# Kernel tuning notes

Measured on AMD Instinct MI355X. Metric: run time of the kernel, lower is better.

The kernel has to match this reference:

```python
import jax, jax.numpy as jnp
import numpy as np

B, L, H, E = 2, 2048, 8, 64
S = L  # self-attention


def setup_inputs() -> dict:
    key = jax.random.key(0)
    k1, k2, k3, k4, k5 = jax.random.split(key, 5)
    return {
        "queries": jax.random.normal(k1, (B, L, H, E), dtype=jnp.float32),
        "keys": jax.random.normal(k2, (B, S, H, E), dtype=jnp.float32),
        "values": jax.random.normal(k3, (B, S, H, E), dtype=jnp.float32),
        "tau": jax.random.uniform(k4, (B, 1), dtype=jnp.float32),
        "delta": jax.random.normal(k5, (B, S), dtype=jnp.float32),
    }


def reference(queries, keys, values, tau, delta):
    # De-stationary attention: scores = (QK^T) * tau + delta, causal mask, softmax, AV
    E_ = queries.shape[-1]
    scale = 1.0 / jnp.sqrt(jnp.float32(E_))
    tau_b = tau[:, None, None, :]      # [B,1,1,1]
    delta_b = delta[:, None, None, :]  # [B,1,1,S]
    scores = jnp.einsum('blhe,bshe->bhls', queries, keys) * tau_b + delta_b  # [B,H,L,S]
    Lq, Sk = scores.shape[-2], scores.shape[-1]
    causal = jnp.triu(jnp.ones((Lq, Sk), dtype=bool), k=1)  # True = masked
    scores = jnp.where(causal[None, None], -jnp.inf, scores)
    A = jax.nn.softmax(scale * scores, axis=-1)
    V = jnp.einsum('bhls,bshd->blhd', A, values)
    return V
```

## Files before the change

### kernel.cpp

```cpp
#include <hip/hip_runtime.h>


typedef _Float16 h8 __attribute__((ext_vector_type(8)));
typedef _Float16 h2 __attribute__((ext_vector_type(2)));
typedef float f32x4 __attribute__((ext_vector_type(4)));

constexpr int Bc = 2, Lc = 2048, Hc = 8, Ec = 64, Sc = 2048;
constexpr int QTL = 128;
constexpr int NQT = Lc / QTL;
constexpr int KT = 64;
constexpr int NBH = Bc * Hc;
constexpr int CH = 8;
constexpr int EPB = 40;
constexpr int NIT = NBH * EPB;
constexpr float SCALE = 0.125f;
constexpr float LOG2E = 1.44269504088896340736f;

__constant__ int d_qtbase[16] = {0,1,2,3,4,6,8,10,12,15,18,21,24,28,32,36};
__constant__ signed char d_eqt[40] = {
  15,15,15,15,
  14,14,14,
  13,13,13,
  12,12,12,
  11,11,11,
  10,10,
   9, 9,
   8, 8,
   7, 7,
   6,
   5,
   4,
   3,
  14,10, 6, 2,
  13, 9, 5, 1,
  12, 8, 4, 0};
__constant__ signed char d_ec0[40] = {
   0, 1, 2, 3,
   0, 1, 2,
   0, 1, 2,
   0, 1, 2,
   0, 1, 2,
   0, 1,
   0, 1,
   0, 1,
   0, 1,
   0,
   0,
   0,
   0,
   3, 2, 1, 0,
   3, 2, 1, 0,
   3, 2, 1, 0};

__device__ __forceinline__ h2 pk2(float x, float y) {
  return __builtin_bit_cast(h2, __builtin_amdgcn_cvt_pkrtz(x, y));
}
template <int CTRL>
__device__ __forceinline__ float dpp_f(float x) {
  int r = __builtin_amdgcn_update_dpp(0, __builtin_bit_cast(int, x), CTRL, 0xF, 0xF, true);
  return __builtin_bit_cast(float, r);
}
__device__ __forceinline__ void gl16(const void* g, void* l) {
  __builtin_amdgcn_global_load_lds(
      (const __attribute__((address_space(1))) void*)g,
      (__attribute__((address_space(3))) void*)l, 16, 0, 0);
}

__global__ __launch_bounds__(256, 4)
void dsattn_prep(const float* __restrict__ Kg, const float* __restrict__ Vg,
                 _Float16* __restrict__ Kh, _Float16* __restrict__ Vh) {
  __shared__ __align__(16) _Float16 T[64][72];
  const int kt = (int)blockIdx.x;
  const int bh = (int)blockIdx.y;
  const int b = bh >> 3, h = bh & 7;
  const int tid = (int)threadIdx.x;
  const int sr = tid >> 2;
  const int e0 = (tid & 3) << 4;
  const int s = kt * KT + sr;

  {
    const float* kp = Kg + (((size_t)b * Sc + s) * Hc + h) * Ec + e0;
    float4 a0 = ((const float4*)kp)[0], a1 = ((const float4*)kp)[1];
    float4 a2 = ((const float4*)kp)[2], a3 = ((const float4*)kp)[3];
    union { h8 v; h2 c[4]; } u0, u1;
    u0.c[0] = pk2(a0.x, a0.y); u0.c[1] = pk2(a0.z, a0.w);
    u0.c[2] = pk2(a1.x, a1.y); u0.c[3] = pk2(a1.z, a1.w);
    u1.c[0] = pk2(a2.x, a2.y); u1.c[1] = pk2(a2.z, a2.w);
    u1.c[2] = pk2(a3.x, a3.y); u1.c[3] = pk2(a3.z, a3.w);
    char* out = (char*)Kh + (((size_t)bh * Sc + s) << 7);
    const int sl = e0 >> 3;
    const int rx = (sr & 7) << 4;
    *(h8*)(out + ((sl << 4) ^ rx)) = u0.v;
    *(h8*)(out + (((sl + 1) << 4) ^ rx)) = u1.v;
  }

  {
    const float* vp = Vg + (((size_t)b * Sc + s) * Hc + h) * Ec + e0;
    float4 v0 = ((const float4*)vp)[0], v1 = ((const float4*)vp)[1];
    float4 v2 = ((const float4*)vp)[2], v3 = ((const float4*)vp)[3];
    const float ev[16] = {v0.x, v0.y, v0.z, v0.w, v1.x, v1.y, v1.z, v1.w,
                          v2.x, v2.y, v2.z, v2.w, v3.x, v3.y, v3.z, v3.w};
#pragma unroll
    for (int j = 0; j < 8; ++j) {
      h2 t = pk2(ev[2 * j], ev[2 * j + 1]);
      T[e0 + 2 * j][sr] = t[0];
      T[e0 + 2 * j + 1][sr] = t[1];
    }
  }
  __syncthreads();
  {
    const int er = tid >> 2;
    const int k0 = (tid & 3) << 4;
    h8 w0 = *(const h8*)&T[er][k0];
    h8 w1 = *(const h8*)&T[er][k0 + 8];
    char* out = (char*)Vh + (((size_t)bh * 32 + kt) << 13) + er * 128;
    const int sl = k0 >> 3;
    const int rx = (er & 7) << 4;
    *(h8*)(out + ((sl << 4) ^ rx)) = w0;
    *(h8*)(out + (((sl + 1) << 4) ^ rx)) = w1;
  }
}

__global__ __launch_bounds__(256, 3)
void dsattn_fwd_main(const float* __restrict__ Qg, const _Float16* __restrict__ Kh,
                     const _Float16* __restrict__ Vh, const float* __restrict__ taug,
                     const float* __restrict__ deltag, float* __restrict__ Og,
                     _Float16* __restrict__ Opart, float* __restrict__ Lpart) {
  __shared__ __align__(16) _Float16 Ks[2][KT * 64];
  __shared__ __align__(16) _Float16 Vt[2][Ec * 64];
  __shared__ __align__(16) _Float16 Pb[4][16 * 64];

  const int tid = (int)threadIdx.x;
  const int wave = tid >> 6, lane = tid & 63;
  const int quad = lane >> 4, l16 = lane & 15;
  _Float16* pb = &Pb[wave][0];
  const int lo = l16 & 1;
  const int pbase = (lo ? 32 : 0) + (l16 & ~1);
  const int kx = (l16 & 7) << 3;
  const int koff0 = (quad * 8) ^ kx;
  const int koff1 = (quad * 8 + 32) ^ kx;

  h8 onesf;
#pragma unroll
  for (int j = 0; j < 8; ++j) onesf[j] = (_Float16)1.0f;

  for (int it = (int)blockIdx.x; it < NIT; it += (int)gridDim.x) {
    const int xcd = it & 7;
    const int r_ = it >> 3;
    const int bh = (xcd << 1) | (r_ & 1);
    const int e = r_ >> 1;
    const int qt = d_eqt[e], c0 = d_ec0[e];
    const int ntiles = 2 * qt + 2;
    const int nch = (ntiles + CH - 1) / CH;
    const int ktBeg = c0 * CH;
    const int ktEnd = min(ktBeg + CH - 1, ntiles - 1);
    const int q0 = qt * QTL;
    const int b = bh >> 3, h = bh & 7;
    const float ct = taug[b] * (SCALE * LOG2E);

    h8 qfrag[2][2];
#pragma unroll
    for (int f = 0; f < 2; ++f)
#pragma unroll
      for (int kk = 0; kk < 2; ++kk) {
        const float* qp = Qg + (((size_t)b * Lc + q0 + 32 * wave + 16 * f + l16) * Hc + h) * Ec
                         + quad * 8 + kk * 32;
        const float4* p = (const float4*)qp;
        union { h8 v; h2 c[4]; } u;
        float4 a0 = p[0], a1 = p[1];
        u.c[0] = pk2(a0.x, a0.y); u.c[1] = pk2(a0.z, a0.w);
        u.c[2] = pk2(a1.x, a1.y); u.c[3] = pk2(a1.z, a1.w);
        qfrag[f][kk] = u.v;
      }

    f32x4 Oacc[2][4], Osum[2];
#pragma unroll
    for (int f = 0; f < 2; ++f) {
#pragma unroll
      for (int nt = 0; nt < 4; ++nt) Oacc[f][nt] = (f32x4){0.f, 0.f, 0.f, 0.f};
      Osum[f] = (f32x4){0.f, 0.f, 0.f, 0.f};
    }
    float dcur[4];

    __syncthreads();

    {
      const char* kg = (const char*)Kh + (((size_t)bh * Sc + (size_t)ktBeg * KT) << 7)
                       + wave * 2048 + lane * 16;
      const char* vg = (const char*)Vh + (((size_t)bh * 32 + ktBeg) << 13)
                       + wave * 2048 + lane * 16;
      char* kl = (char*)&Ks[0][0] + wave * 2048;
      char* vl = (char*)&Vt[0][0] + wave * 2048;
      gl16(kg, kl); gl16(kg + 1024, kl + 1024);
      gl16(vg, vl); gl16(vg + 1024, vl + 1024);
#pragma unroll
      for (int nt = 0; nt < 4; ++nt)
        dcur[nt] = deltag[(size_t)b * Sc + ktBeg * KT + nt * 16 + l16] * (SCALE * LOG2E);
    }

    for (int kt = ktBeg; kt <= ktEnd; ++kt) {
      const int cur = (kt - ktBeg) & 1;
      const bool pf = (kt < ktEnd);
      const int kbase = kt * KT;

      __syncthreads();

      float dn[4];
      if (pf) {
        const char* kg = (const char*)Kh + (((size_t)bh * Sc + (size_t)(kt + 1) * KT) << 7)
                         + wave * 2048 + lane * 16;
        const char* vg = (const char*)Vh + (((size_t)bh * 32 + kt + 1) << 13)
                         + wave * 2048 + lane * 16;
        char* kl = (char*)&Ks[cur ^ 1][0] + wave * 2048;
        char* vl = (char*)&Vt[cur ^ 1][0] + wave * 2048;
        gl16(kg, kl); gl16(kg + 1024, kl + 1024);
        gl16(vg, vl); gl16(vg + 1024, vl + 1024);
#pragma unroll
        for (int nt = 0; nt < 4; ++nt)
          dn[nt] = deltag[(size_t)b * Sc + (kt + 1) * KT + nt * 16 + l16];
      }

      const int wtop = q0 + 32 * wave + 31;
      if (kbase <= wtop) {
#pragma unroll
        for (int f = 0; f < 2; ++f) {
          f32x4 Sacc[4];
#pragma unroll
          for (int nt = 0; nt < 4; ++nt) Sacc[nt] = (f32x4){0.f, 0.f, 0.f, 0.f};
          __builtin_amdgcn_s_setprio(1);
#pragma unroll
          for (int kk = 0; kk < 2; ++kk) {
            const int ko = kk ? koff1 : koff0;
            h8 bf[4];
#pragma unroll
            for (int nt = 0; nt < 4; ++nt)
              bf[nt] = *(const h8*)&Ks[cur][(nt * 16 + l16) * 64 + ko];
#pragma unroll
            for (int nt = 0; nt < 4; ++nt)
              Sacc[nt] = __builtin_amdgcn_mfma_f32_16x16x32_f16(qfrag[f][kk], bf[nt], Sacc[nt], 0, 0, 0);
          }
          __builtin_amdgcn_s_setprio(0);

          const int fr0 = q0 + 32 * wave + 16 * f;
#pragma unroll
          for (int nt = 0; nt < 4; ++nt)
#pragma unroll
            for (int rr = 0; rr < 4; ++rr)
              Sacc[nt][rr] = Sacc[nt][rr] * ct + dcur[nt];
          if (kbase + 63 > fr0) {
#pragma unroll
            for (int nt = 0; nt < 4; ++nt) {
              const int key = kbase + nt * 16 + l16;
#pragma unroll
              for (int rr = 0; rr < 4; ++rr)
                if (key > fr0 + quad * 4 + rr) Sacc[nt][rr] = -1e30f;
            }
          }
#pragma unroll
          for (int nt = 0; nt < 4; ++nt)
#pragma unroll
            for (int rr = 0; rr < 4; ++rr)
              Sacc[nt][rr] = __builtin_amdgcn_exp2f(Sacc[nt][rr]);

#pragma unroll
          for (int rr = 0; rr < 4; ++rr) {
            float o0 = dpp_f<0xB1>(Sacc[0][rr]);
            float o1 = dpp_f<0xB1>(Sacc[1][rr]);
            float o2 = dpp_f<0xB1>(Sacc[2][rr]);
            float o3 = dpp_f<0xB1>(Sacc[3][rr]);
            h2 d0 = lo ? pk2(o2, Sacc[2][rr]) : pk2(Sacc[0][rr], o0);
            h2 d1 = lo ? pk2(o3, Sacc[3][rr]) : pk2(Sacc[1][rr], o1);
            const int row = (quad << 2) + rr;
            char* pr = (char*)pb + row * 128;
            const int rx = (row & 7) << 4;
            *(h2*)(pr + ((pbase * 2) ^ rx)) = d0;
            *(h2*)(pr + ((pbase * 2 + 32) ^ rx)) = d1;
          }
          asm volatile("s_waitcnt lgkmcnt(0)" ::: "memory");
          __builtin_amdgcn_sched_barrier(0);

          h8 af0 = *(const h8*)&pb[l16 * 64 + koff0];
          h8 af1 = *(const h8*)&pb[l16 * 64 + koff1];

          __builtin_amdgcn_s_setprio(1);
#pragma unroll
          for (int nt = 0; nt < 4; ++nt) {
            h8 vf0 = *(const h8*)&Vt[cur][(nt * 16 + l16) * 64 + koff0];
            Oacc[f][nt] = __builtin_amdgcn_mfma_f32_16x16x32_f16(af0, vf0, Oacc[f][nt], 0, 0, 0);
            h8 vf1 = *(const h8*)&Vt[cur][(nt * 16 + l16) * 64 + koff1];
            Oacc[f][nt] = __builtin_amdgcn_mfma_f32_16x16x32_f16(af1, vf1, Oacc[f][nt], 0, 0, 0);
          }
          Osum[f] = __builtin_amdgcn_mfma_f32_16x16x32_f16(af0, onesf, Osum[f], 0, 0, 0);
          Osum[f] = __builtin_amdgcn_mfma_f32_16x16x32_f16(af1, onesf, Osum[f], 0, 0, 0);
          __builtin_amdgcn_s_setprio(0);
        }
      }

      if (pf) {
#pragma unroll
        for (int nt = 0; nt < 4; ++nt) dcur[nt] = dn[nt] * (SCALE * LOG2E);
      }
    }

    if (nch == 1) {
#pragma unroll
      for (int f = 0; f < 2; ++f)
#pragma unroll
        for (int rr = 0; rr < 4; ++rr) {
          const int qrow = q0 + 32 * wave + 16 * f + (quad << 2) + rr;
          const float inv = 1.0f / Osum[f][rr];
          float* op = Og + (((size_t)b * Lc + qrow) * Hc + h) * Ec;
#pragma unroll
          for (int nt = 0; nt < 4; ++nt) op[nt * 16 + l16] = Oacc[f][nt][rr] * inv;
        }
    } else {
      const int en = bh * EPB + d_qtbase[qt] + c0;
      _Float16* op = Opart + (size_t)en * (QTL * Ec);
#pragma unroll
      for (int f = 0; f < 2; ++f)
#pragma unroll
        for (int rr = 0; rr < 4; ++rr) {
          const int row = 32 * wave + 16 * f + (quad << 2) + rr;
#pragma unroll
          for (int nt = 0; nt < 4; ++nt)
            op[row * Ec + nt * 16 + l16] = (_Float16)Oacc[f][nt][rr];
          if (l16 == 0) Lpart[en * QTL + row] = Osum[f][rr];
        }
    }
  }
}

__global__ __launch_bounds__(256, 4)
void dsattn_comb_main(const _Float16* __restrict__ Opart, const float* __restrict__ Lpart,
                      float* __restrict__ Og) {
  const int qt = (CH / 2) + ((int)blockIdx.x >> 2);
  const int slab = (int)blockIdx.x & 3;
  const int bh = (int)blockIdx.y;
  const int b = bh >> 3, h = bh & 7;
  const int nch = (2 * qt + 1 + CH) / CH;
  const int e0 = bh * EPB + d_qtbase[qt];
  const int row = slab * 32 + ((int)threadIdx.x >> 3);
  const int col = ((int)threadIdx.x & 7) << 3;

  float acc[8];
#pragma unroll
  for (int i = 0; i < 8; ++i) acc[i] = 0.f;
  float l = 0.f;
  for (int c = 0; c < nch; ++c) {
    l += Lpart[(e0 + c) * QTL + row];
    h8 v = *(const h8*)(Opart + (size_t)(e0 + c) * (QTL * Ec) + row * Ec + col);
#pragma unroll
    for (int i = 0; i < 8; ++i) acc[i] += (float)v[i];
  }
  const float inv = 1.0f / l;
  float* out = Og + (((size_t)b * Lc + qt * QTL + row) * Hc + h) * Ec + col;
  float4 o0, o1;
  o0.x = acc[0] * inv; o0.y = acc[1] * inv; o0.z = acc[2] * inv; o0.w = acc[3] * inv;
  o1.x = acc[4] * inv; o1.y = acc[5] * inv; o1.z = acc[6] * inv; o1.w = acc[7] * inv;
  ((float4*)out)[0] = o0;
  ((float4*)out)[1] = o1;
}

__global__ __launch_bounds__(256, 2)
void dsattn_fwd_mono(const float* __restrict__ Qg, const float* __restrict__ Kg,
                     const float* __restrict__ Vg, const float* __restrict__ taug,
                     const float* __restrict__ deltag, float* __restrict__ Og) {
  constexpr int LDK = 72;
  __shared__ __align__(16) _Float16 Ks[2][KT * LDK];
  __shared__ __align__(16) _Float16 Vt[2][Ec * LDK];
  __shared__ __align__(16) _Float16 Pb[4][16 * LDK];

  const int tid = (int)threadIdx.x;
  const int wave = tid >> 6, lane = tid & 63;
  const int quad = lane >> 4, l16 = lane & 15;
  const int srow = tid >> 2;
  const int sec = (tid & 3) << 4;
  const int vrp = ((tid >> 3) + 4 * (tid & 7)) & 31;
  const int ve8 = (tid & 7) << 3;
  _Float16* pb = &Pb[wave][0];
  const int lo = l16 & 1;
  const int pbase = (lo ? 32 : 0) + (l16 & ~1);

  h8 onesf;
#pragma unroll
  for (int j = 0; j < 8; ++j) onesf[j] = (_Float16)1.0f;

  for (int wid = (int)blockIdx.x; wid < NQT * NBH; wid += (int)gridDim.x) {
    const int bh = wid & (NBH - 1);
    const int qt = NQT - 1 - (wid >> 4);
    const int ktEnd = 2 * qt + 1;
    const int q0 = qt * QTL;
    const int b = bh >> 3, h = bh & 7;
    const float ct = taug[b] * (SCALE * LOG2E);

    h8 qfrag[2][2];
#pragma unroll
    for (int f = 0; f < 2; ++f)
#pragma unroll
      for (int kk = 0; kk < 2; ++kk) {
        const float* qp = Qg + (((size_t)b * Lc + q0 + 32 * wave + 16 * f + l16) * Hc + h) * Ec
                         + quad * 8 + kk * 32;
        const float4* p = (const float4*)qp;
        union { h8 v; h2 c[4]; } u;
        float4 a0 = p[0], a1 = p[1];
        u.c[0] = pk2(a0.x, a0.y); u.c[1] = pk2(a0.z, a0.w);
        u.c[2] = pk2(a1.x, a1.y); u.c[3] = pk2(a1.z, a1.w);
        qfrag[f][kk] = u.v;
      }

    f32x4 Oacc[2][4], Osum[2];
#pragma unroll
    for (int f = 0; f < 2; ++f) {
#pragma unroll
      for (int nt = 0; nt < 4; ++nt) Oacc[f][nt] = (f32x4){0.f, 0.f, 0.f, 0.f};
      Osum[f] = (f32x4){0.f, 0.f, 0.f, 0.f};
    }
    float dcur[4];

    __syncthreads();

    {
      const float* kp = Kg + (((size_t)b * Sc + srow) * Hc + h) * Ec + sec;
      float4 c0v = ((const float4*)kp)[0], c1v = ((const float4*)kp)[1];
      float4 c2v = ((const float4*)kp)[2], c3v = ((const float4*)kp)[3];
      const float* vp0 = Vg + (((size_t)b * Sc + 2 * vrp) * Hc + h) * Ec + ve8;
      const float* vp1 = vp0 + Hc * Ec;
      float4 r00 = ((const float4*)vp0)[0], r01 = ((const float4*)vp0)[1];
      float4 r10 = ((const float4*)vp1)[0], r11 = ((const float4*)vp1)[1];
#pragma unroll
      for (int nt = 0; nt < 4; ++nt)
        dcur[nt] = deltag[(size_t)b * Sc + nt * 16 + l16] * (SCALE * LOG2E);
      union { h8 v; h2 c[4]; } w0, w1;
      w0.c[0] = pk2(c0v.x, c0v.y); w0.c[1] = pk2(c0v.z, c0v.w);
      w0.c[2] = pk2(c1v.x, c1v.y); w0.c[3] = pk2(c1v.z, c1v.w);
      w1.c[0] = pk2(c2v.x, c2v.y); w1.c[1] = pk2(c2v.z, c2v.w);
      w1.c[2] = pk2(c3v.x, c3v.y); w1.c[3] = pk2(c3v.z, c3v.w);
      *(h8*)&Ks[0][srow * LDK + sec] = w0.v;
      *(h8*)&Ks[0][srow * LDK + sec + 8] = w1.v;
      const float e0[8] = {r00.x, r00.y, r00.z, r00.w, r01.x, r01.y, r01.z, r01.w};
      const float e1[8] = {r10.x, r10.y, r10.z, r10.w, r11.x, r11.y, r11.z, r11.w};
#pragma unroll
      for (int j = 0; j < 8; ++j)
        *(h2*)&Vt[0][(ve8 + j) * LDK + 2 * vrp] = pk2(e0[j], e1[j]);
    }

    for (int kt = 0; kt <= ktEnd; ++kt) {
      const int cur = kt & 1;
      const bool pf = (kt < ktEnd);
      const int kbase = kt * KT;

      __syncthreads();

      float4 kn0, kn1, kn2, kn3, vn00, vn01, vn10, vn11;
      float dn[4];
      if (pf) {
        const int nb = (kt + 1) * KT;
        const float* kp = Kg + (((size_t)b * Sc + nb + srow) * Hc + h) * Ec + sec;
        kn0 = ((const float4*)kp)[0]; kn1 = ((const float4*)kp)[1];
        kn2 = ((const float4*)kp)[2]; kn3 = ((const float4*)kp)[3];
        const float* vp0 = Vg + (((size_t)b * Sc + nb + 2 * vrp) * Hc + h) * Ec + ve8;
        const float* vp1 = vp0 + Hc * Ec;
        vn00 = ((const float4*)vp0)[0]; vn01 = ((const float4*)vp0)[1];
        vn10 = ((const float4*)vp1)[0]; vn11 = ((const float4*)vp1)[1];
#pragma unroll
        for (int nt = 0; nt < 4; ++nt)
          dn[nt] = deltag[(size_t)b * Sc + nb + nt * 16 + l16];
      }

      const int wtop = q0 + 32 * wave + 31;
      if (kbase <= wtop) {
        f32x4 Sacc[2][4];
#pragma unroll
        for (int f = 0; f < 2; ++f)
#pragma unroll
          for (int nt = 0; nt < 4; ++nt) Sacc[f][nt] = (f32x4){0.f, 0.f, 0.f, 0.f};
#pragma unroll
        for (int kk = 0; kk < 2; ++kk) {
          h8 bf[4];
#pragma unroll
          for (int nt = 0; nt < 4; ++nt)
            bf[nt] = *(const h8*)&Ks[cur][(nt * 16 + l16) * LDK + quad * 8 + kk * 32];
#pragma unroll
          for (int f = 0; f < 2; ++f)
#pragma unroll
            for (int nt = 0; nt < 4; ++nt)
              Sacc[f][nt] = __builtin_amdgcn_mfma_f32_16x16x32_f16(qfrag[f][kk], bf[nt], Sacc[f][nt], 0, 0, 0);
        }

#pragma unroll
        for (int f = 0; f < 2; ++f) {
          const int fr0 = q0 + 32 * wave + 16 * f;
          float sv[4][4];
#pragma unroll
          for (int nt = 0; nt < 4; ++nt)
#pragma unroll
            for (int rr = 0; rr < 4; ++rr)
              sv[nt][rr] = Sacc[f][nt][rr] * ct + dcur[nt];
          if (kbase + 63 > fr0) {
#pragma unroll
            for (int nt = 0; nt < 4; ++nt) {
              const int key = kbase + nt * 16 + l16;
#pragma unroll
              for (int rr = 0; rr < 4; ++rr)
                if (key > fr0 + quad * 4 + rr) sv[nt][rr] = -1e30f;
            }
          }
#pragma unroll
          for (int nt = 0; nt < 4; ++nt)
#pragma unroll
            for (int rr = 0; rr < 4; ++rr)
              sv[nt][rr] = __builtin_amdgcn_exp2f(sv[nt][rr]);

#pragma unroll
          for (int rr = 0; rr < 4; ++rr) {
            float o0 = dpp_f<0xB1>(sv[0][rr]);
            float o1 = dpp_f<0xB1>(sv[1][rr]);
            float o2 = dpp_f<0xB1>(sv[2][rr]);
            float o3 = dpp_f<0xB1>(sv[3][rr]);
            h2 d0 = lo ? pk2(o2, sv[2][rr]) : pk2(sv[0][rr], o0);
            h2 d1 = lo ? pk2(o3, sv[3][rr]) : pk2(sv[1][rr], o1);
            _Float16* pp = &pb[((quad << 2) + rr) * LDK + pbase];
            *(h2*)pp = d0;
            *(h2*)(pp + 16) = d1;
          }
          asm volatile("s_waitcnt lgkmcnt(0)" ::: "memory");

          h8 af0 = *(const h8*)&pb[l16 * LDK + quad * 8];
          h8 af1 = *(const h8*)&pb[l16 * LDK + quad * 8 + 32];

#pragma unroll
          for (int nt = 0; nt < 4; ++nt) {
            h8 vf0 = *(const h8*)&Vt[cur][(nt * 16 + l16) * LDK + quad * 8];
            Oacc[f][nt] = __builtin_amdgcn_mfma_f32_16x16x32_f16(af0, vf0, Oacc[f][nt], 0, 0, 0);
            h8 vf1 = *(const h8*)&Vt[cur][(nt * 16 + l16) * LDK + quad * 8 + 32];
            Oacc[f][nt] = __builtin_amdgcn_mfma_f32_16x16x32_f16(af1, vf1, Oacc[f][nt], 0, 0, 0);
          }
          Osum[f] = __builtin_amdgcn_mfma_f32_16x16x32_f16(af0, onesf, Osum[f], 0, 0, 0);
          Osum[f] = __builtin_amdgcn_mfma_f32_16x16x32_f16(af1, onesf, Osum[f], 0, 0, 0);
        }
      }

      if (pf) {
        _Float16* ksn = &Ks[cur ^ 1][0];
        _Float16* vtn = &Vt[cur ^ 1][0];
        union { h8 v; h2 c[4]; } w0, w1;
        w0.c[0] = pk2(kn0.x, kn0.y); w0.c[1] = pk2(kn0.z, kn0.w);
        w0.c[2] = pk2(kn1.x, kn1.y); w0.c[3] = pk2(kn1.z, kn1.w);
        w1.c[0] = pk2(kn2.x, kn2.y); w1.c[1] = pk2(kn2.z, kn2.w);
        w1.c[2] = pk2(kn3.x, kn3.y); w1.c[3] = pk2(kn3.z, kn3.w);
        *(h8*)&ksn[srow * LDK + sec] = w0.v;
        *(h8*)&ksn[srow * LDK + sec + 8] = w1.v;
        const float e0[8] = {vn00.x, vn00.y, vn00.z, vn00.w, vn01.x, vn01.y, vn01.z, vn01.w};
        const float e1[8] = {vn10.x, vn10.y, vn10.z, vn10.w, vn11.x, vn11.y, vn11.z, vn11.w};
#pragma unroll
        for (int j = 0; j < 8; ++j)
          *(h2*)&vtn[(ve8 + j) * LDK + 2 * vrp] = pk2(e0[j], e1[j]);
#pragma unroll
        for (int nt = 0; nt < 4; ++nt) dcur[nt] = dn[nt] * (SCALE * LOG2E);
      }
    }

#pragma unroll
    for (int f = 0; f < 2; ++f)
#pragma unroll
      for (int rr = 0; rr < 4; ++rr) {
        const int qrow = q0 + 32 * wave + 16 * f + (quad << 2) + rr;
        const float inv = 1.0f / Osum[f][rr];
        float* op = Og + (((size_t)b * Lc + qrow) * Hc + h) * Ec;
#pragma unroll
        for (int nt = 0; nt < 4; ++nt) op[nt * 16 + l16] = Oacc[f][nt][rr] * inv;
      }
  }
}

extern "C" void kernel_launch(void* const* d_in, const int* in_sizes, int n_in,
                              void* d_out, int out_size, void* d_ws, size_t ws_size,
                              hipStream_t stream) {
  const float* Q = (const float*)d_in[0];
  const float* K = (const float*)d_in[1];
  const float* V = (const float*)d_in[2];
  const float* tau = (const float*)d_in[3];
  const float* delta = (const float*)d_in[4];
  float* O = (float*)d_out;

  const size_t needOp = (size_t)NIT * QTL * Ec * 2;
  const size_t needLp = (size_t)NIT * QTL * 4;
  const size_t needKh = (size_t)NBH * Sc * Ec * 2;
  const size_t needVh = needKh;
  const size_t need = needOp + needLp + needKh + needVh;

  if (ws_size >= need) {
    _Float16* Opart = (_Float16*)d_ws;
    float* Lpart = (float*)((char*)d_ws + needOp);
    _Float16* Kh = (_Float16*)((char*)d_ws + needOp + needLp);
    _Float16* Vh = (_Float16*)((char*)d_ws + needOp + needLp + needKh);
    dsattn_prep<<<dim3(Sc / KT, NBH), 256, 0, stream>>>(K, V, Kh, Vh);
    dsattn_fwd_main<<<dim3(NIT), 256, 0, stream>>>(Q, Kh, Vh, tau, delta, O, Opart, Lpart);
    dsattn_comb_main<<<dim3((NQT - CH / 2) * 4, NBH), 256, 0, stream>>>(Opart, Lpart, O);
  } else {
    dsattn_fwd_mono<<<dim3(NQT * NBH), 256, 0, stream>>>(Q, K, V, tau, delta, O);
  }
}
```

Before: 107.0 us.

## Fuse split-KV combine into main kernel via last-arriver atomic counter

```diff
diff --git a/kernel.cpp b/kernel.cpp
--- a/kernel.cpp
+++ b/kernel.cpp
@@ -18,37 +18,15 @@
 
 __constant__ int d_qtbase[16] = {0,1,2,3,4,6,8,10,12,15,18,21,24,28,32,36};
 __constant__ signed char d_eqt[40] = {
-  15,15,15,15,
-  14,14,14,
-  13,13,13,
-  12,12,12,
-  11,11,11,
-  10,10,
-   9, 9,
-   8, 8,
-   7, 7,
-   6,
-   5,
-   4,
-   3,
+  15,15,15,15, 14,14,14, 13,13,13, 12,12,12, 11,11,11,
   14,10, 6, 2,
+  10,10, 9, 9, 8, 8, 7, 7, 6, 5, 4, 3,
   13, 9, 5, 1,
   12, 8, 4, 0};
 __constant__ signed char d_ec0[40] = {
-   0, 1, 2, 3,
-   0, 1, 2,
-   0, 1, 2,
-   0, 1, 2,
-   0, 1, 2,
-   0, 1,
-   0, 1,
-   0, 1,
-   0, 1,
-   0,
-   0,
-   0,
-   0,
+   0, 1, 2, 3,  0, 1, 2,  0, 1, 2,  0, 1, 2,  0, 1, 2,
    3, 2, 1, 0,
+   0, 1, 0, 1, 0, 1, 0, 1, 0, 0, 0, 0,
    3, 2, 1, 0,
    3, 2, 1, 0};
 
@@ -68,7 +46,8 @@
 
 __global__ __launch_bounds__(256, 4)
 void dsattn_prep(const float* __restrict__ Kg, const float* __restrict__ Vg,
-                 _Float16* __restrict__ Kh, _Float16* __restrict__ Vh) {
+                 _Float16* __restrict__ Kh, _Float16* __restrict__ Vh,
+                 int* __restrict__ cnt) {
   __shared__ __align__(16) _Float16 T[64][72];
   const int kt = (int)blockIdx.x;
   const int bh = (int)blockIdx.y;
@@ -77,6 +56,8 @@
   const int sr = tid >> 2;
   const int e0 = (tid & 3) << 4;
   const int s = kt * KT + sr;
+
+  if (kt == 0 && tid < NQT) cnt[bh * NQT + tid] = 0;
 
   {
     const float* kp = Kg + (((size_t)b * Sc + s) * Hc + h) * Ec + e0;
@@ -125,7 +106,8 @@
 void dsattn_fwd_main(const float* __restrict__ Qg, const _Float16* __restrict__ Kh,
                      const _Float16* __restrict__ Vh, const float* __restrict__ taug,
                      const float* __restrict__ deltag, float* __restrict__ Og,
-                     _Float16* __restrict__ Opart, float* __restrict__ Lpart) {
+                     _Float16* __restrict__ Opart, float* __restrict__ Lpart,
+                     int* __restrict__ cnt) {
   __shared__ __align__(16) _Float16 Ks[2][KT * 64];
   __shared__ __align__(16) _Float16 Vt[2][Ec * 64];
   __shared__ __align__(16) _Float16 Pb[4][16 * 64];
@@ -314,7 +296,8 @@
           for (int nt = 0; nt < 4; ++nt) op[nt * 16 + l16] = Oacc[f][nt][rr] * inv;
         }
     } else {
-      const int en = bh * EPB + d_qtbase[qt] + c0;
+      const int base = bh * EPB + d_qtbase[qt];
+      const int en = base + c0;
       _Float16* op = Opart + (size_t)en * (QTL * Ec);
 #pragma unroll
       for (int f = 0; f < 2; ++f)
@@ -326,39 +309,43 @@
             op[row * Ec + nt * 16 + l16] = (_Float16)Oacc[f][nt][rr];
           if (l16 == 0) Lpart[en * QTL + row] = Osum[f][rr];
         }
+
+      volatile int* s_flag = (volatile int*)&Pb[0][0];
+      __threadfence();
+      __syncthreads();
+      if (tid == 0) {
+        int old = atomicAdd(&cnt[bh * NQT + qt], 1);
+        *s_flag = (old == nch - 1) ? 1 : 0;
+      }
+      __syncthreads();
+      if (*s_flag) {
+        __threadfence();
+        const int row0 = tid >> 3;
+        const int col = (tid & 7) << 3;
+#pragma unroll
+        for (int slab = 0; slab < 4; ++slab) {
+          const int row = slab * 32 + row0;
+          float acc[8];
+#pragma unroll
+          for (int i = 0; i < 8; ++i) acc[i] = 0.f;
+          float l = 0.f;
+          for (int c = 0; c < nch; ++c) {
+            l += Lpart[(base + c) * QTL + row];
+            h8 v = *(const h8*)(Opart + (size_t)(base + c) * (QTL * Ec) + row * Ec + col);
+#pragma unroll
+            for (int i = 0; i < 8; ++i) acc[i] += (float)v[i];
+          }
+          const float inv = 1.0f / l;
+          float* out = Og + (((size_t)b * Lc + q0 + row) * Hc + h) * Ec + col;
+          float4 o0, o1;
+          o0.x = acc[0] * inv; o0.y = acc[1] * inv; o0.z = acc[2] * inv; o0.w = acc[3] * inv;
+          o1.x = acc[4] * inv; o1.y = acc[5] * inv; o1.z = acc[6] * inv; o1.w = acc[7] * inv;
+          ((float4*)out)[0] = o0;
+          ((float4*)out)[1] = o1;
+        }
+      }
     }
   }
-}
-
-__global__ __launch_bounds__(256, 4)
-void dsattn_comb_main(const _Float16* __restrict__ Opart, const float* __restrict__ Lpart,
-                      float* __restrict__ Og) {
-  const int qt = (CH / 2) + ((int)blockIdx.x >> 2);
-  const int slab = (int)blockIdx.x & 3;
-  const int bh = (int)blockIdx.y;
-  const int b = bh >> 3, h = bh & 7;
-  const int nch = (2 * qt + 1 + CH) / CH;
-  const int e0 = bh * EPB + d_qtbase[qt];
-  const int row = slab * 32 + ((int)threadIdx.x >> 3);
-  const int col = ((int)threadIdx.x & 7) << 3;
-
-  float acc[8];
-#pragma unroll
-  for (int i = 0; i < 8; ++i) acc[i] = 0.f;
-  float l = 0.f;
-  for (int c = 0; c < nch; ++c) {
-    l += Lpart[(e0 + c) * QTL + row];
-    h8 v = *(const h8*)(Opart + (size_t)(e0 + c) * (QTL * Ec) + row * Ec + col);
-#pragma unroll
-    for (int i = 0; i < 8; ++i) acc[i] += (float)v[i];
-  }
-  const float inv = 1.0f / l;
-  float* out = Og + (((size_t)b * Lc + qt * QTL + row) * Hc + h) * Ec + col;
-  float4 o0, o1;
-  o0.x = acc[0] * inv; o0.y = acc[1] * inv; o0.z = acc[2] * inv; o0.w = acc[3] * inv;
-  o1.x = acc[4] * inv; o1.y = acc[5] * inv; o1.z = acc[6] * inv; o1.w = acc[7] * inv;
-  ((float4*)out)[0] = o0;
-  ((float4*)out)[1] = o1;
 }
 
 __global__ __launch_bounds__(256, 2)
@@ -587,16 +574,18 @@
   const size_t needLp = (size_t)NIT * QTL * 4;
   const size_t needKh = (size_t)NBH * Sc * Ec * 2;
   const size_t needVh = needKh;
-  const size_t need = needOp + needLp + needKh + needVh;
+  const size_t needCnt = (size_t)NBH * NQT * 4;
+  const size_t need = needOp + needLp + needKh + needVh + needCnt;
 
   if (ws_size >= need) {
     _Float16* Opart = (_Float16*)d_ws;
     float* Lpart = (float*)((char*)d_ws + needOp);
     _Float16* Kh = (_Float16*)((char*)d_ws + needOp + needLp);
     _Float16* Vh = (_Float16*)((char*)d_ws + needOp + needLp + needKh);
-    dsattn_prep<<<dim3(Sc / KT, NBH), 256, 0, stream>>>(K, V, Kh, Vh);
-    dsattn_fwd_main<<<dim3(NIT), 256, 0, stream>>>(Q, Kh, Vh, tau, delta, O, Opart, Lpart);
-    dsattn_comb_main<<<dim3((NQT - CH / 2) * 4, NBH), 256, 0, stream>>>(Opart, Lpart, O);
+    int* cnt = (int*)((char*)d_ws + needOp + needLp + needKh + needVh);
+    dsattn_prep<<<dim3(Sc / KT, NBH), 256, 0, stream>>>(K, V, Kh, Vh, cnt);
+    dsattn_fwd_main<<<dim3(NIT), 256, 0, stream>>>(Q, Kh, Vh, tau, delta, O,
+                                                   Opart, Lpart, cnt);
   } else {
     dsattn_fwd_mono<<<dim3(NQT * NBH), 256, 0, stream>>>(Q, K, V, tau, delta, O);
   }
```

Result: slower. 197.5 us (+84.5%).

## Pack partial outputs as fp16 quads and reorder split-KV work schedule

Applied to the files above, without the earlier changes.

```diff
diff --git a/kernel.cpp b/kernel.cpp
--- a/kernel.cpp
+++ b/kernel.cpp
@@ -18,37 +18,15 @@
 
 __constant__ int d_qtbase[16] = {0,1,2,3,4,6,8,10,12,15,18,21,24,28,32,36};
 __constant__ signed char d_eqt[40] = {
-  15,15,15,15,
-  14,14,14,
-  13,13,13,
-  12,12,12,
-  11,11,11,
-  10,10,
-   9, 9,
-   8, 8,
-   7, 7,
-   6,
-   5,
-   4,
-   3,
+  15,15,15,15, 14,14,14, 13,13,13, 12,12,12, 11,11,11,
   14,10, 6, 2,
+  10,10, 9, 9, 8, 8, 7, 7, 6, 5, 4, 3,
   13, 9, 5, 1,
   12, 8, 4, 0};
 __constant__ signed char d_ec0[40] = {
-   0, 1, 2, 3,
-   0, 1, 2,
-   0, 1, 2,
-   0, 1, 2,
-   0, 1, 2,
-   0, 1,
-   0, 1,
-   0, 1,
-   0, 1,
-   0,
-   0,
-   0,
-   0,
+   0, 1, 2, 3,  0, 1, 2,  0, 1, 2,  0, 1, 2,  0, 1, 2,
    3, 2, 1, 0,
+   0, 1, 0, 1, 0, 1, 0, 1, 0, 0, 0, 0,
    3, 2, 1, 0,
    3, 2, 1, 0};
 
@@ -321,9 +299,12 @@
 #pragma unroll
         for (int rr = 0; rr < 4; ++rr) {
           const int row = 32 * wave + 16 * f + (quad << 2) + rr;
-#pragma unroll
-          for (int nt = 0; nt < 4; ++nt)
-            op[row * Ec + nt * 16 + l16] = (_Float16)Oacc[f][nt][rr];
+          h2 a = pk2(Oacc[f][0][rr], Oacc[f][1][rr]);
+          h2 bq = pk2(Oacc[f][2][rr], Oacc[f][3][rr]);
+          uint2 w;
+          w.x = __builtin_bit_cast(unsigned, a);
+          w.y = __builtin_bit_cast(unsigned, bq);
+          *(uint2*)(op + ((size_t)row * 16 + l16) * 4) = w;
           if (l16 == 0) Lpart[en * QTL + row] = Osum[f][rr];
         }
     }
@@ -339,26 +320,28 @@
   const int b = bh >> 3, h = bh & 7;
   const int nch = (2 * qt + 1 + CH) / CH;
   const int e0 = bh * EPB + d_qtbase[qt];
-  const int row = slab * 32 + ((int)threadIdx.x >> 3);
-  const int col = ((int)threadIdx.x & 7) << 3;
-
-  float acc[8];
-#pragma unroll
-  for (int i = 0; i < 8; ++i) acc[i] = 0.f;
-  float l = 0.f;
-  for (int c = 0; c < nch; ++c) {
-    l += Lpart[(e0 + c) * QTL + row];
-    h8 v = *(const h8*)(Opart + (size_t)(e0 + c) * (QTL * Ec) + row * Ec + col);
-#pragma unroll
-    for (int i = 0; i < 8; ++i) acc[i] += (float)v[i];
-  }
-  const float inv = 1.0f / l;
-  float* out = Og + (((size_t)b * Lc + qt * QTL + row) * Hc + h) * Ec + col;
-  float4 o0, o1;
-  o0.x = acc[0] * inv; o0.y = acc[1] * inv; o0.z = acc[2] * inv; o0.w = acc[3] * inv;
-  o1.x = acc[4] * inv; o1.y = acc[5] * inv; o1.z = acc[6] * inv; o1.w = acc[7] * inv;
-  ((float4*)out)[0] = o0;
-  ((float4*)out)[1] = o1;
+  const int l16 = (int)threadIdx.x & 15;
+  const int rg = (int)threadIdx.x >> 4;
+
+#pragma unroll
+  for (int rr = 0; rr < 2; ++rr) {
+    const int row = slab * 32 + rg * 2 + rr;
+    float acc[4] = {0.f, 0.f, 0.f, 0.f};
+    float l = 0.f;
+    for (int c = 0; c < nch; ++c) {
+      l += Lpart[(e0 + c) * QTL + row];
+      uint2 w = *(const uint2*)(Opart + (size_t)(e0 + c) * (QTL * Ec)
+                                + ((size_t)row * 16 + l16) * 4);
+      h2 a = __builtin_bit_cast(h2, w.x);
+      h2 bq = __builtin_bit_cast(h2, w.y);
+      acc[0] += (float)a[0]; acc[1] += (float)a[1];
+      acc[2] += (float)bq[0]; acc[3] += (float)bq[1];
+    }
+    const float inv = 1.0f / l;
+    float* out = Og + (((size_t)b * Lc + qt * QTL + row) * Hc + h) * Ec;
+#pragma unroll
+    for (int nt = 0; nt < 4; ++nt) out[nt * 16 + l16] = acc[nt] * inv;
+  }
 }
 
 __global__ __launch_bounds__(256, 2)
@@ -595,7 +578,8 @@
     _Float16* Kh = (_Float16*)((char*)d_ws + needOp + needLp);
     _Float16* Vh = (_Float16*)((char*)d_ws + needOp + needLp + needKh);
     dsattn_prep<<<dim3(Sc / KT, NBH), 256, 0, stream>>>(K, V, Kh, Vh);
-    dsattn_fwd_main<<<dim3(NIT), 256, 0, stream>>>(Q, Kh, Vh, tau, delta, O, Opart, Lpart);
+    dsattn_fwd_main<<<dim3(NIT), 256, 0, stream>>>(Q, Kh, Vh, tau, delta, O,
+                                                   Opart, Lpart);
     dsattn_comb_main<<<dim3((NQT - CH / 2) * 4, NBH), 256, 0, stream>>>(Opart, Lpart, O);
   } else {
     dsattn_fwd_mono<<<dim3(NQT * NBH), 256, 0, stream>>>(Q, K, V, tau, delta, O);
```

New measurement: 107.0 us (median of 3 runs). Within noise of the previous version (+0.0%).
